# Kernel optimization log

Hardware: AMD Instinct MI355X
Metric: run time of the kernel (lower is better)

Reference implementation:

```python
import jax, jax.numpy as jnp
import numpy as np

N = 50000      # num_nodes
E = 500000     # num_edges
D_IN = 128     # in_features
D_OUT = 128    # out_features
D_REL = 128    # nrela_dim
NEG_SLOPE = 0.2   # LeakyReLU alpha
RATIO = 0.5       # float ratio -> simple (non-schedule) branch
LN_EPS = 1e-5


def setup_inputs() -> dict:
    key = jax.random.key(0)
    ks = jax.random.split(key, 8)
    edge_index = jax.random.randint(ks[0], (2, E), 0, N, dtype=jnp.int64)
    x = jax.random.normal(ks[1], (N, D_IN), dtype=jnp.float32)
    edge_type_embed = jax.random.normal(ks[2], (E, D_REL), dtype=jnp.float32)
    # learned params (xavier-ish scale)
    W = jax.random.normal(ks[3], (4, 2 * D_OUT + D_REL, D_OUT), dtype=jnp.float32) * 0.05
    a = jax.random.normal(ks[4], (4, D_OUT, 1), dtype=jnp.float32) * 0.05
    xw = jax.random.normal(ks[5], (D_IN, D_OUT), dtype=jnp.float32) * (1.0 / np.sqrt(D_IN))
    xb = jnp.zeros((D_OUT,), dtype=jnp.float32)
    gamma = jnp.ones((D_OUT,), dtype=jnp.float32)
    beta = jnp.zeros((D_OUT,), dtype=jnp.float32)
    return {"edge_index": edge_index, "x": x, "edge_type_embed": edge_type_embed,
            "W": W, "a": a, "xw": xw, "xb": xb, "gamma": gamma, "beta": beta}


def _segment_softmax(score, seg, num_segments):
    # per-source-node softmax over edges (matches torch_geometric softmax util)
    seg_max = jax.ops.segment_max(score, seg, num_segments=num_segments)
    seg_max = jnp.where(jnp.isfinite(seg_max), seg_max, 0.0)  # empty segments
    e = jnp.exp(score - seg_max[seg])
    denom = jax.ops.segment_sum(e, seg, num_segments=num_segments)
    return e / (denom[seg] + 1e-16)


def _one_iter(edge_index, xc, ete, Wi, ai):
    src, dst = edge_index[0], edge_index[1]
    # [E, 2*D_OUT + D_REL] @ [2*D_OUT+D_REL, D_OUT] -> [E, D_OUT]
    edge_h = jnp.concatenate([xc[src], xc[dst], ete], axis=1) @ Wi
    score = jax.nn.leaky_relu(jnp.squeeze(edge_h @ ai, -1), NEG_SLOPE)  # [E]
    alpha = _segment_softmax(score, src, N)
    k = int(E * RATIO)
    _, idx = jax.lax.top_k(alpha, k)
    mask = jnp.zeros((E,), dtype=bool).at[idx].set(True)
    alpha = jnp.where(mask, alpha, 0.0)
    # scatter-add weighted messages back to source nodes
    return jax.ops.segment_sum(alpha[:, None] * edge_h, src, num_segments=N)


def reference(edge_index, x, edge_type_embed, W, a, xw, xb, gamma, beta):
    xc = x @ xw + xb  # x_linear
    for i in range(4):  # fixed 4 aggregation iterations (float-ratio branch)
        xc = _one_iter(edge_index, xc, edge_type_embed, W[i], a[i])
    xc = jax.nn.elu(xc)  # concat=True
    mu = jnp.mean(xc, axis=-1, keepdims=True)
    var = jnp.var(xc, axis=-1, keepdims=True)
    return (xc - mu) * jax.lax.rsqrt(var + LN_EPS) * gamma + beta
```

## Files before the change

### kernel.cpp

```cpp
#include <hip/hip_runtime.h>
#include <math.h>

#define DOUT 128

typedef unsigned short u16;
typedef __attribute__((ext_vector_type(8))) short bf16x8;
typedef __attribute__((ext_vector_type(4))) float f32x4;

static __device__ __forceinline__ f32x4 mfma16x16x32(bf16x8 a, bf16x8 b, f32x4 c) {
  return __builtin_amdgcn_mfma_f32_16x16x32_bf16(a, b, c, 0, 0, 0);
}

static __device__ __forceinline__ short bf16i(int v) {
  return (short)(__float_as_uint((float)v) >> 16);
}

static __device__ __forceinline__ float wsum64(float v) {
#pragma unroll
  for (int off = 32; off > 0; off >>= 1) v += __shfl_xor(v, off, 64);
  return v;
}
static __device__ __forceinline__ float wmax64(float v) {
#pragma unroll
  for (int off = 32; off > 0; off >>= 1) v = fmaxf(v, __shfl_xor(v, off, 64));
  return v;
}
static __device__ __forceinline__ float rsumg(float v) {
  v += __shfl_xor(v, 16, 64);
  v += __shfl_xor(v, 32, 64);
  return v;
}

static __device__ __forceinline__ void split3(float x, u16& h, u16& m, u16& l) {
  unsigned u = __float_as_uint(x);
  unsigned rh = u + 0x7FFFu + ((u >> 16) & 1u);
  h = (u16)(rh >> 16);
  float hf = __uint_as_float(rh & 0xFFFF0000u);
  float d1 = x - hf;
  unsigned v = __float_as_uint(d1);
  unsigned rm = v + 0x7FFFu + ((v >> 16) & 1u);
  m = (u16)(rm >> 16);
  float mf = __uint_as_float(rm & 0xFFFF0000u);
  float d2 = d1 - mf;
  unsigned w2 = __float_as_uint(d2);
  unsigned rl = w2 + 0x7FFFu + ((w2 >> 16) & 1u);
  l = (u16)(rl >> 16);
}

static __device__ __forceinline__ void split34(float4 v, uint2& h, uint2& m, uint2& lo) {
  u16 h0, h1, h2, h3, m0, m1, m2, m3, l0, l1, l2, l3;
  split3(v.x, h0, m0, l0);
  split3(v.y, h1, m1, l1);
  split3(v.z, h2, m2, l2);
  split3(v.w, h3, m3, l3);
  h.x = (unsigned)h0 | ((unsigned)h1 << 16);
  h.y = (unsigned)h2 | ((unsigned)h3 << 16);
  m.x = (unsigned)m0 | ((unsigned)m1 << 16);
  m.y = (unsigned)m2 | ((unsigned)m3 << 16);
  lo.x = (unsigned)l0 | ((unsigned)l1 << 16);
  lo.y = (unsigned)l2 | ((unsigned)l3 << 16);
}

__global__ void zero_kernel(int* __restrict__ degcur, unsigned* __restrict__ hists,
                            unsigned* __restrict__ rep, int* __restrict__ candcnt4, int N) {
  int i = blockIdx.x * blockDim.x + threadIdx.x;
  if (i < N) degcur[i] = 0;
  if (i < 4096) hists[i] = 0u;
  if (i < 32768) rep[i] = 0u;
  if (i < 4) candcnt4[i] = 0;
}

__global__ void detect_kernel(const void* __restrict__ ei, int* __restrict__ flag, int E) {
  const int* p = (const int*)ei;
  int lim = (E < 65536) ? E : 65536;
  int i = blockIdx.x * blockDim.x + threadIdx.x;
  int any = 0;
  for (; i < lim; i += gridDim.x * blockDim.x) any |= (p[2 * i + 1] != 0);
  if (__any(any))
    if ((threadIdx.x & 63) == 0 && any) atomicOr(flag, 1);
}

__global__ void cvt_deg_kernel(const void* __restrict__ ei, const int* __restrict__ flag,
                               int* __restrict__ src, int* __restrict__ dst,
                               int* __restrict__ degcur, int E) {
  int i = blockIdx.x * blockDim.x + threadIdx.x;
  if (i >= E) return;
  int s, d;
  if (*flag) { const int* p = (const int*)ei; s = p[i]; d = p[E + i]; }
  else { const long long* p = (const long long*)ei; s = (int)p[i]; d = (int)p[(size_t)E + i]; }
  src[i] = s;
  dst[i] = d;
  atomicAdd(&degcur[s], 1);
}

__global__ void scan_rowptr_kernel(int* __restrict__ degcur, int* __restrict__ rowptr, int N) {
  const int tid = threadIdx.x;
  const int lane = tid & 63, wid = tid >> 6;
  __shared__ int wsumS[16];
  __shared__ int sbase;
  if (tid == 0) sbase = 0;
  __syncthreads();
  for (int base = 0; base < N; base += 1024) {
    int i = base + tid;
    int v = (i < N) ? degcur[i] : 0;
    int x = v;
#pragma unroll
    for (int off = 1; off < 64; off <<= 1) {
      int y = __shfl_up(x, off, 64);
      if (lane >= off) x += y;
    }
    if (lane == 63) wsumS[wid] = x;
    __syncthreads();
    int wbase = 0;
#pragma unroll
    for (int w2 = 0; w2 < 16; ++w2) wbase += (w2 < wid) ? wsumS[w2] : 0;
    int excl = sbase + wbase + x - v;
    if (i < N) { rowptr[i] = excl; degcur[i] = excl; }
    __syncthreads();
    if (tid == 1023) sbase += wbase + x;
    __syncthreads();
  }
  if (tid == 0) rowptr[N] = sbase;
}

__global__ void scatter_kernel(const int* __restrict__ src, int* __restrict__ cursor,
                               int* __restrict__ eids, int E) {
  int e = blockIdx.x * blockDim.x + threadIdx.x;
  if (e >= E) return;
  int p = atomicAdd(&cursor[src[e]], 1);
  eids[p] = e;
}

__global__ void sort_eids_kernel(const int* __restrict__ rowptr, int* __restrict__ eids, int N) {
  int n = blockIdx.x * blockDim.x + threadIdx.x;
  if (n >= N) return;
  int p0 = rowptr[n], p1 = rowptr[n + 1];
  for (int i = p0 + 1; i < p1; ++i) {
    int key = eids[i];
    int j = i - 1;
    while (j >= p0 && eids[j] > key) { eids[j + 1] = eids[j]; --j; }
    eids[j + 1] = key;
  }
}

__global__ void wa_all_kernel(const float* __restrict__ W, const float* __restrict__ a,
                              float* __restrict__ wa_all) {
  int it = blockIdx.x;
  int k = threadIdx.x;
  const float* row = W + ((size_t)it * 384 + k) * DOUT;
  const float* ai = a + (size_t)it * DOUT;
  float acc = 0.f;
  for (int j = 0; j < DOUT; ++j) acc = fmaf(row[j], ai[j], acc);
  wa_all[it * 384 + k] = acc;
}

__global__ void wsplit_kernel(const float* __restrict__ xw, const float* __restrict__ W,
                              u16* __restrict__ wtH, u16* __restrict__ wtM,
                              u16* __restrict__ wtL) {
  __shared__ int muS[32];
  int tid = threadIdx.x;
  {
    int lw = tid & 63, g = lw >> 4;
    bf16x8 aEnc;
#pragma unroll
    for (int j = 0; j < 8; ++j) aEnc[j] = bf16i(8 * g + j + 1);
    f32x4 z = {0.f, 0.f, 0.f, 0.f};
    for (int t0 = 0; t0 < 32; ++t0) {
      int g0 = t0 >> 3, j0 = t0 & 7;
      bf16x8 bOne;
#pragma unroll
      for (int j = 0; j < 8; ++j)
        bOne[j] = (g == g0 && j == j0) ? (short)0x3F80 : (short)0;
      f32x4 d = mfma16x16x32(aEnc, bOne, z);
      if (tid == t0) muS[t0] = ((int)(d[0] + 0.5f) - 1) & 31;
    }
  }
  __syncthreads();
  int b = blockIdx.x;
  int set, ks;
  const float* srcp;
  if (b < 4) { set = 0; ks = b; srcp = xw; }
  else { set = 1 + (b - 4) / 12; ks = (b - 4) % 12; srcp = W + (size_t)(set - 1) * 384 * DOUT; }
  size_t base = ((size_t)set * 12 + ks) * 4096;
  for (int i = tid; i < 4096; i += blockDim.x) {
    int col = i >> 5, t = i & 31;
    float x = srcp[(size_t)(ks * 32 + muS[t]) * DOUT + col];
    u16 h, m, l;
    split3(x, h, m, l);
    wtH[base + i] = h;
    wtM[base + i] = m;
    wtL[base + i] = l;
  }
}

__global__ __launch_bounds__(256) void et4_kernel(const float* __restrict__ ete,
                                                  const float* __restrict__ wa_all,
                                                  float* __restrict__ et4, int E) {
  __shared__ float4 w3s[4][32];
  int tid = threadIdx.x;
  if (tid < 128) {
    int it = tid >> 5, k4 = tid & 31;
    const float* base = wa_all + it * 384 + 256 + k4 * 4;
    w3s[it][k4] = make_float4(base[0], base[1], base[2], base[3]);
  }
  __syncthreads();
  int e = blockIdx.x * blockDim.x + tid;
  if (e >= E) return;
  const float4* row = (const float4*)(ete + (size_t)e * DOUT);
  float a0 = 0.f, a1 = 0.f, a2 = 0.f, a3 = 0.f;
#pragma unroll
  for (int k4 = 0; k4 < 32; ++k4) {
    float4 r = row[k4];
    float4 w0 = w3s[0][k4], w1 = w3s[1][k4], w2 = w3s[2][k4], w3v = w3s[3][k4];
    a0 = fmaf(r.x, w0.x, fmaf(r.y, w0.y, fmaf(r.z, w0.z, fmaf(r.w, w0.w, a0))));
    a1 = fmaf(r.x, w1.x, fmaf(r.y, w1.y, fmaf(r.z, w1.z, fmaf(r.w, w1.w, a1))));
    a2 = fmaf(r.x, w2.x, fmaf(r.y, w2.y, fmaf(r.z, w2.z, fmaf(r.w, w2.w, a2))));
    a3 = fmaf(r.x, w3v.x, fmaf(r.y, w3v.y, fmaf(r.z, w3v.z, fmaf(r.w, w3v.w, a3))));
  }
  et4[e] = a0;
  et4[(size_t)E + e] = a1;
  et4[(size_t)2 * E + e] = a2;
  et4[(size_t)3 * E + e] = a3;
}

__global__ __launch_bounds__(256) void softmax_kernel(
    const int* __restrict__ rowptr, const int* __restrict__ eids, const int* __restrict__ dst,
    const float* __restrict__ pa, const float* __restrict__ qa, const float* __restrict__ et4,
    int it, int E, float* __restrict__ alpha, unsigned* __restrict__ rep0, int N) {
  __shared__ unsigned lh[256];
  int tid = threadIdx.x;
  lh[tid] = 0u;
  __syncthreads();
  const float* etp = et4 + (size_t)it * E;
  int w = (int)(((size_t)blockIdx.x * blockDim.x + tid) >> 6);
  int lane = tid & 63;
  if (w < N) {
    int p0 = rowptr[w], p1 = rowptr[w + 1];
    int deg = p1 - p0;
    if (deg > 0) {
      float pan = pa[w];
      if (deg <= 64) {
        int p = p0 + lane;
        int e = -1;
        float sv = -3.402823466e38f;
        if (p < p1) {
          e = eids[p];
          float s = pan + qa[dst[e]] + etp[e];
          sv = (s >= 0.f) ? s : 0.2f * s;
        }
        float m = wmax64(sv);
        float ee = (e >= 0) ? expf(sv - m) : 0.f;
        float den = 0.f;
        for (int i = 0; i < deg; ++i) den += __shfl(ee, i, 64);
        den += 1e-16f;
        if (e >= 0) {
          float av = ee / den;
          alpha[e] = av;
          atomicAdd(&lh[__float_as_uint(av) >> 24], 1u);
        }
      } else if (deg <= 256) {
        float sv[4]; int ev[4];
#pragma unroll
        for (int u = 0; u < 4; ++u) {
          int p = p0 + u * 64 + lane;
          if (p < p1) {
            int e = eids[p];
            ev[u] = e;
            float s = pan + qa[dst[e]] + etp[e];
            sv[u] = (s >= 0.f) ? s : 0.2f * s;
          } else { ev[u] = -1; sv[u] = -3.402823466e38f; }
        }
        float m = fmaxf(fmaxf(sv[0], sv[1]), fmaxf(sv[2], sv[3]));
        m = wmax64(m);
        float ssum = 0.f;
#pragma unroll
        for (int u = 0; u < 4; ++u)
          if (ev[u] >= 0) { sv[u] = expf(sv[u] - m); ssum += sv[u]; }
        ssum = wsum64(ssum);
        float den = ssum + 1e-16f;
#pragma unroll
        for (int u = 0; u < 4; ++u)
          if (ev[u] >= 0) {
            float av = sv[u] / den;
            alpha[ev[u]] = av;
            atomicAdd(&lh[__float_as_uint(av) >> 24], 1u);
          }
      } else {
        float m = -3.402823466e38f;
        for (int p = p0 + lane; p < p1; p += 64) {
          int e = eids[p];
          float s = pan + qa[dst[e]] + etp[e];
          s = (s >= 0.f) ? s : 0.2f * s;
          m = fmaxf(m, s);
        }
        m = wmax64(m);
        float ssum = 0.f;
        for (int p = p0 + lane; p < p1; p += 64) {
          int e = eids[p];
          float s = pan + qa[dst[e]] + etp[e];
          s = (s >= 0.f) ? s : 0.2f * s;
          ssum += expf(s - m);
        }
        ssum = wsum64(ssum);
        float den = ssum + 1e-16f;
        for (int p = p0 + lane; p < p1; p += 64) {
          int e = eids[p];
          float s = pan + qa[dst[e]] + etp[e];
          s = (s >= 0.f) ? s : 0.2f * s;
          float av = expf(s - m) / den;
          alpha[e] = av;
          atomicAdd(&lh[__float_as_uint(av) >> 24], 1u);
        }
      }
    }
  }
  __syncthreads();
  if (lh[tid]) atomicAdd(&rep0[(blockIdx.x & 31) * 256 + tid], lh[tid]);
}

__device__ __forceinline__ void scan256_step(const unsigned* __restrict__ hist, unsigned krem_in,
                                             unsigned* lds, unsigned* res,
                                             unsigned& bin, unsigned& krem_out) {
  int t = threadIdx.x;
  if (t < 256) lds[t] = hist[t];
  __syncthreads();
  for (int off = 1; off < 256; off <<= 1) {
    unsigned add = 0u;
    if (t < 256 && t + off < 256) add = lds[t + off];
    __syncthreads();
    if (t < 256) lds[t] += add;
    __syncthreads();
  }
  if (t < 256) {
    unsigned above = (t == 255) ? 0u : lds[t + 1];
    if (lds[t] >= krem_in && above < krem_in) { res[0] = (unsigned)t; res[1] = krem_in - above; }
  }
  __syncthreads();
  bin = res[0];
  krem_out = res[1];
  __syncthreads();
}

__device__ __forceinline__ void chain_scan(const unsigned* __restrict__ hists, int upto,
                                           unsigned Ktop, unsigned* lds, unsigned* res,
                                           unsigned& pref, unsigned& krem) {
  pref = 0u; krem = Ktop;
  for (int l = 0; l < upto; ++l) {
    unsigned bin, k2;
    scan256_step(hists + l * 256, krem, lds, res, bin, k2);
    pref |= bin << (24 - 8 * l);
    krem = k2;
  }
}

__global__ __launch_bounds__(256) void hist1_kernel(const float* __restrict__ alpha,
                                                    const unsigned* __restrict__ rep0,
                                                    unsigned* __restrict__ hists_it,
                                                    unsigned Ktop, int E) {
  __shared__ unsigned lds[256], res2[2], lh[256];
  int t = threadIdx.x;
  unsigned v = 0u;
#pragma unroll
  for (int r = 0; r < 32; ++r) v += rep0[r * 256 + t];
  if (blockIdx.x == 0) hists_it[t] = v;
  lds[t] = v;
  __syncthreads();
  for (int off = 1; off < 256; off <<= 1) {
    unsigned add = (t + off < 256) ? lds[t + off] : 0u;
    __syncthreads();
    lds[t] += add;
    __syncthreads();
  }
  {
    unsigned above = (t == 255) ? 0u : lds[t + 1];
    if (lds[t] >= Ktop && above < Ktop) { res2[0] = (unsigned)t; res2[1] = Ktop - above; }
  }
  __syncthreads();
  unsigned bin0 = res2[0];
  lh[t] = 0u;
  __syncthreads();
  unsigned* myh = hists_it + 256;
  for (int e = blockIdx.x * blockDim.x + t; e < E; e += gridDim.x * blockDim.x) {
    unsigned b = __float_as_uint(alpha[e]);
    if ((b >> 24) == bin0) atomicAdd(&lh[(b >> 16) & 0xFFu], 1u);
  }
  __syncthreads();
  if (lh[t]) atomicAdd(&myh[t], lh[t]);
}

__global__ void hist_kernel(const float* __restrict__ alpha, unsigned* __restrict__ hists_it,
                            int level, unsigned Ktop, int E) {
  __shared__ unsigned lds[256], res2[2], lh[256];
  unsigned pref = 0u, krem = Ktop;
  if (level > 0) chain_scan(hists_it, level, Ktop, lds, res2, pref, krem);
  int t = threadIdx.x;
  lh[t] = 0u;
  __syncthreads();
  unsigned* myh = hists_it + level * 256;
  int hs = (level > 0) ? (32 - 8 * level) : 0;
  int bs = 24 - 8 * level;
  for (int e = blockIdx.x * blockDim.x + t; e < E; e += gridDim.x * blockDim.x) {
    unsigned b = __float_as_uint(alpha[e]);
    if (level == 0 || (b >> hs) == (pref >> hs)) atomicAdd(&lh[(b >> bs) & 0xFFu], 1u);
  }
  __syncthreads();
  if (lh[t]) atomicAdd(&myh[t], lh[t]);
}

__global__ void hist3c_kernel(const float* __restrict__ alpha, unsigned* __restrict__ hists_it,
                              unsigned Ktop, int* __restrict__ candList,
                              int* __restrict__ candCnt, int E) {
  __shared__ unsigned lds[256], res2[2], lh[256];
  unsigned pref, krem;
  chain_scan(hists_it, 3, Ktop, lds, res2, pref, krem);
  int t = threadIdx.x;
  lh[t] = 0u;
  __syncthreads();
  unsigned* myh = hists_it + 3 * 256;
  for (int e = blockIdx.x * blockDim.x + t; e < E; e += gridDim.x * blockDim.x) {
    unsigned b = __float_as_uint(alpha[e]);
    if ((b >> 8) == (pref >> 8)) {
      atomicAdd(&lh[b & 0xFFu], 1u);
      int p = atomicAdd(candCnt, 1);
      if (p < 4096) candList[p] = e;
    }
  }
  __syncthreads();
  if (lh[t]) atomicAdd(&myh[t], lh[t]);
}

__global__ __launch_bounds__(1024) void resolve24_kernel(
    const float* __restrict__ alpha, float* __restrict__ amask,
    const unsigned* __restrict__ hists_it, unsigned Ktop,
    const int* __restrict__ candList, const int* __restrict__ candCnt,
    int* __restrict__ header, int E) {
  __shared__ unsigned lds[256], res2[2];
  unsigned thr, needU;
  chain_scan(hists_it, 4, Ktop, lds, res2, thr, needU);
  int needT = (int)needU;
  int cc = *candCnt;
  int tid = threadIdx.x;
  __shared__ int tiel[4096];
  __shared__ int tiec;
  if (tid == 0) tiec = 0;
  __syncthreads();
  if (cc <= 4096) {
    for (int i = tid; i < cc; i += blockDim.x) {
      int e = candList[i];
      if (__float_as_uint(alpha[e]) == thr) { int p = atomicAdd(&tiec, 1); tiel[p] = e; }
    }
    __syncthreads();
    int ce = tiec;
    int dropc = ce - needT;
    if (dropc <= 0) {
      if (tid == 0) { header[0] = 0; header[1] = (int)thr; header[2] = 0; }
      return;
    }
    if (dropc <= 64) {
      int sortN = 64;
      while (sortN < ce) sortN <<= 1;
      for (int i = tid; i < sortN; i += blockDim.x)
        if (i >= ce) tiel[i] = 0x7fffffff;
      __syncthreads();
      for (int k = 2; k <= sortN; k <<= 1) {
        for (int j = k >> 1; j > 0; j >>= 1) {
          for (int i = tid; i < sortN; i += blockDim.x) {
            int ixj = i ^ j;
            if (ixj > i) {
              int v0 = tiel[i], v1 = tiel[ixj];
              bool up = ((i & k) == 0);
              if ((v0 > v1) == up) { tiel[i] = v1; tiel[ixj] = v0; }
            }
          }
          __syncthreads();
        }
      }
      if (tid == 0) { header[0] = 0; header[1] = (int)thr; header[2] = dropc; }
      for (int i = tid; i < dropc; i += blockDim.x) header[3 + i] = tiel[needT + i];
      return;
    }
  }
  if (tid == 0) { header[0] = 1; }
  __shared__ int wtot[16];
  __shared__ int sbase;
  if (tid == 0) sbase = 0;
  __syncthreads();
  int lane = tid & 63, wid = tid >> 6;
  for (int base = 0; base < E; base += 1024) {
    int e = base + tid;
    float a = 0.f; int f = 0; unsigned b = 0u;
    if (e < E) { a = alpha[e]; b = __float_as_uint(a); f = (b == thr) ? 1 : 0; }
    int x = f;
#pragma unroll
    for (int off = 1; off < 64; off <<= 1) {
      int y = __shfl_up(x, off, 64);
      if (lane >= off) x += y;
    }
    if (lane == 63) wtot[wid] = x;
    __syncthreads();
    int wbase = 0;
#pragma unroll
    for (int w2 = 0; w2 < 16; ++w2) wbase += (w2 < wid) ? wtot[w2] : 0;
    if (e < E) {
      float outv = 0.f;
      if (b > thr) outv = a;
      else if (f && (sbase + wbase + x - f) < needT) outv = a;
      amask[e] = outv;
    }
    __syncthreads();
    if (tid == 1023) sbase += wbase + x;
    __syncthreads();
  }
}

static __device__ __forceinline__ float edge_w(const float* __restrict__ alpha,
                                               const float* __restrict__ amask,
                                               const int* __restrict__ hdr, int flg,
                                               unsigned thr, int dc, int e) {
  if (flg) return amask[e];
  float av = alpha[e];
  unsigned b = __float_as_uint(av);
  if (b > thr) return av;
  if (b == thr) {
    for (int j = 0; j < dc; ++j)
      if (hdr[3 + j] == e) return 0.f;
    return av;
  }
  return 0.f;
}

__global__ void agg_kernel(const int* __restrict__ rowptr, const int* __restrict__ eids,
                           const int* __restrict__ dst, const float* __restrict__ alpha,
                           const float* __restrict__ amask, const int* __restrict__ hdr,
                           const float* __restrict__ xc, const float* __restrict__ ete,
                           float* __restrict__ sa, float* __restrict__ vbuf,
                           float* __restrict__ tbuf, int N) {
  int w = (int)(((size_t)blockIdx.x * blockDim.x + threadIdx.x) >> 6);
  int lane = threadIdx.x & 63;
  if (w >= N) return;
  const int flg = hdr[0];
  const unsigned thr = (unsigned)hdr[1];
  const int dc = hdr[2];
  int p0 = rowptr[w], p1 = rowptr[w + 1];
  int deg = p1 - p0;
  const int half = lane >> 5;
  const int l32 = lane & 31;
  const float4* xc4 = (const float4*)xc;
  const float4* et4p = (const float4*)ete;
  float4 acc = make_float4(0.f, 0.f, 0.f, 0.f);
  float s = 0.f;
  if (deg <= 64) {
    int p = p0 + lane;
    int e = -1; float am = 0.f; int dd = 0;
    if (p < p1) { e = eids[p]; am = edge_w(alpha, amask, hdr, flg, thr, dc, e); dd = dst[e]; }
    for (int i = 0; i < deg; ++i) {
      float a = __shfl(am, i, 64);
      if (a != 0.f) {
        int ei = __shfl(e, i, 64);
        int di = __shfl(dd, i, 64);
        const float4* b = half ? (et4p + (size_t)ei * 32) : (xc4 + (size_t)di * 32);
        float4 r = b[l32];
        acc.x = fmaf(a, r.x, acc.x); acc.y = fmaf(a, r.y, acc.y);
        acc.z = fmaf(a, r.z, acc.z); acc.w = fmaf(a, r.w, acc.w);
        s += a;
      }
    }
  } else {
    for (int p = p0; p < p1; ++p) {
      int e0 = eids[p];
      float a0 = edge_w(alpha, amask, hdr, flg, thr, dc, e0);
      if (a0 != 0.f) {
        int d0 = dst[e0];
        const float4* b0 = half ? (et4p + (size_t)e0 * 32) : (xc4 + (size_t)d0 * 32);
        float4 r = b0[l32];
        acc.x = fmaf(a0, r.x, acc.x); acc.y = fmaf(a0, r.y, acc.y);
        acc.z = fmaf(a0, r.z, acc.z); acc.w = fmaf(a0, r.w, acc.w);
        s += a0;
      }
    }
  }
  if (half == 0) ((float4*)vbuf)[(size_t)w * 32 + l32] = acc;
  else           ((float4*)tbuf)[(size_t)w * 32 + l32] = acc;
  if (lane == 0) sa[w] = s;
}

__global__ __launch_bounds__(256) void gemm_mfma_kernel(
    const float* __restrict__ A0, const float* __restrict__ A1, const float* __restrict__ A2,
    const float* __restrict__ sca, const u16* __restrict__ wtH, const u16* __restrict__ wtM,
    const u16* __restrict__ wtL, const float* __restrict__ bias, float* __restrict__ C,
    int N, int nseg,
    const float* __restrict__ wa_next, float* __restrict__ pa, float* __restrict__ qa,
    const float* __restrict__ gamma, const float* __restrict__ beta,
    float* __restrict__ outp, int epi) {
  __shared__ __align__(16) char smem[61440];
  u16 (*AsH)[40] = (u16(*)[40])(smem);
  u16 (*AsM)[40] = (u16(*)[40])(smem + 10240);
  u16 (*AsL)[40] = (u16(*)[40])(smem + 20480);
  u16 (*BsH)[40] = (u16(*)[40])(smem + 30720);
  u16 (*BsM)[40] = (u16(*)[40])(smem + 40960);
  u16 (*BsL)[40] = (u16(*)[40])(smem + 51200);
  const int tid = threadIdx.x;
  const int m0 = blockIdx.x * 128;
  const int K = DOUT * nseg;
  const int w = tid >> 6, l = tid & 63;
  const int cb = l & 15, g = l >> 4;

  int rowlab[4], collab[4];
  {
    bf16x8 enc, ones;
#pragma unroll
    for (int j = 0; j < 8; ++j) { enc[j] = bf16i(cb + 1); ones[j] = (short)0x3F80; }
    f32x4 z = {0.f, 0.f, 0.f, 0.f};
    f32x4 dR = mfma16x16x32(enc, ones, z);
    f32x4 dC = mfma16x16x32(ones, enc, z);
#pragma unroll
    for (int r = 0; r < 4; ++r) {
      rowlab[r] = ((int)(dR[r] * (1.f / 32.f) + 0.5f) - 1) & 15;
      collab[r] = ((int)(dC[r] * (1.f / 32.f) + 0.5f) - 1) & 15;
    }
  }

  f32x4 acc[2][8];
#pragma unroll
  for (int i = 0; i < 2; ++i)
#pragma unroll
    for (int j = 0; j < 8; ++j) acc[i][j] = (f32x4){0.f, 0.f, 0.f, 0.f};

  const int srow = tid >> 1, shalf = tid & 1;
  const int grow_s = m0 + srow;
  float scv = 1.f;
  if (sca && grow_s < N) scv = sca[grow_s];

  for (int kc = 0; kc < K; kc += 32) {
    const int seg = kc >> 7;
    const float* Ap = (seg == 0) ? A0 : (seg == 1) ? A1 : A2;
    float4 v0 = make_float4(0.f, 0.f, 0.f, 0.f), v1 = v0, v2 = v0, v3 = v0;
    if (grow_s < N) {
      const float4* p = (const float4*)(Ap + (size_t)grow_s * DOUT + (kc & 127) + shalf * 16);
      v0 = p[0]; v1 = p[1]; v2 = p[2]; v3 = p[3];
      if (seg == 0 && sca) {
        v0.x *= scv; v0.y *= scv; v0.z *= scv; v0.w *= scv;
        v1.x *= scv; v1.y *= scv; v1.z *= scv; v1.w *= scv;
        v2.x *= scv; v2.y *= scv; v2.z *= scv; v2.w *= scv;
        v3.x *= scv; v3.y *= scv; v3.z *= scv; v3.w *= scv;
      }
    }
    uint2 h0, m0v, l0, h1, m1v, l1, h2, m2v, l2, h3, m3v, l3;
    split34(v0, h0, m0v, l0); split34(v1, h1, m1v, l1);
    split34(v2, h2, m2v, l2); split34(v3, h3, m3v, l3);
    *(uint4*)&AsH[srow][shalf * 16]     = make_uint4(h0.x, h0.y, h1.x, h1.y);
    *(uint4*)&AsH[srow][shalf * 16 + 8] = make_uint4(h2.x, h2.y, h3.x, h3.y);
    *(uint4*)&AsM[srow][shalf * 16]     = make_uint4(m0v.x, m0v.y, m1v.x, m1v.y);
    *(uint4*)&AsM[srow][shalf * 16 + 8] = make_uint4(m2v.x, m2v.y, m3v.x, m3v.y);
    *(uint4*)&AsL[srow][shalf * 16]     = make_uint4(l0.x, l0.y, l1.x, l1.y);
    *(uint4*)&AsL[srow][shalf * 16 + 8] = make_uint4(l2.x, l2.y, l3.x, l3.y);
    {
      size_t sb = (size_t)(kc >> 5) << 12;
      const uint4* gh = (const uint4*)(wtH + sb) + tid * 2;
      const uint4* gm = (const uint4*)(wtM + sb) + tid * 2;
      const uint4* gl = (const uint4*)(wtL + sb) + tid * 2;
      uint4 bh0 = gh[0], bh1 = gh[1];
      uint4 bm0 = gm[0], bm1 = gm[1];
      uint4 bl0 = gl[0], bl1 = gl[1];
      *(uint4*)&BsH[srow][shalf * 16]     = bh0;
      *(uint4*)&BsH[srow][shalf * 16 + 8] = bh1;
      *(uint4*)&BsM[srow][shalf * 16]     = bm0;
      *(uint4*)&BsM[srow][shalf * 16 + 8] = bm1;
      *(uint4*)&BsL[srow][shalf * 16]     = bl0;
      *(uint4*)&BsL[srow][shalf * 16 + 8] = bl1;
    }
    __syncthreads();
    bf16x8 aH0 = *(const bf16x8*)&AsH[w * 32 + cb][g * 8];
    bf16x8 aH1 = *(const bf16x8*)&AsH[w * 32 + 16 + cb][g * 8];
    bf16x8 aM0 = *(const bf16x8*)&AsM[w * 32 + cb][g * 8];
    bf16x8 aM1 = *(const bf16x8*)&AsM[w * 32 + 16 + cb][g * 8];
    bf16x8 aL0 = *(const bf16x8*)&AsL[w * 32 + cb][g * 8];
    bf16x8 aL1 = *(const bf16x8*)&AsL[w * 32 + 16 + cb][g * 8];
#pragma unroll
    for (int ct = 0; ct < 8; ++ct) {
      bf16x8 bH = *(const bf16x8*)&BsH[ct * 16 + cb][g * 8];
      bf16x8 bM = *(const bf16x8*)&BsM[ct * 16 + cb][g * 8];
      bf16x8 bL = *(const bf16x8*)&BsL[ct * 16 + cb][g * 8];
      acc[0][ct] = mfma16x16x32(aH0, bH, acc[0][ct]);
      acc[1][ct] = mfma16x16x32(aH1, bH, acc[1][ct]);
      acc[0][ct] = mfma16x16x32(aM0, bH, acc[0][ct]);
      acc[1][ct] = mfma16x16x32(aM1, bH, acc[1][ct]);
      acc[0][ct] = mfma16x16x32(aL0, bH, acc[0][ct]);
      acc[1][ct] = mfma16x16x32(aL1, bH, acc[1][ct]);
      acc[0][ct] = mfma16x16x32(aH0, bM, acc[0][ct]);
      acc[1][ct] = mfma16x16x32(aH1, bM, acc[1][ct]);
      acc[0][ct] = mfma16x16x32(aM0, bM, acc[0][ct]);
      acc[1][ct] = mfma16x16x32(aM1, bM, acc[1][ct]);
      acc[0][ct] = mfma16x16x32(aH0, bL, acc[0][ct]);
      acc[1][ct] = mfma16x16x32(aH1, bL, acc[1][ct]);
    }
    __syncthreads();
  }

  float* slab = (float*)(smem + (size_t)w * 8448);
  const int row16 = l & 15;
  const int csel = (l >> 4) * 32;
#pragma unroll
  for (int rt = 0; rt < 2; ++rt) {
#pragma unroll
    for (int ct = 0; ct < 8; ++ct)
#pragma unroll
      for (int r = 0; r < 4; ++r)
        slab[rowlab[r] * 132 + ct * 16 + collab[r]] = acc[rt][ct][r];
    __syncthreads();
    int grow = m0 + w * 32 + rt * 16 + row16;
    float v[32];
#pragma unroll
    for (int q = 0; q < 8; ++q) {
      float4 t4 = *(float4*)&slab[row16 * 132 + csel + q * 4];
      v[q * 4 + 0] = t4.x; v[q * 4 + 1] = t4.y; v[q * 4 + 2] = t4.z; v[q * 4 + 3] = t4.w;
    }
    if (bias) {
#pragma unroll
      for (int q = 0; q < 8; ++q) {
        float4 bb = *(const float4*)(bias + csel + q * 4);
        v[q * 4 + 0] += bb.x; v[q * 4 + 1] += bb.y; v[q * 4 + 2] += bb.z; v[q * 4 + 3] += bb.w;
      }
    }
    if (epi == 2) {
#pragma unroll
      for (int i = 0; i < 32; ++i) v[i] = (v[i] > 0.f) ? v[i] : expm1f(v[i]);
      float s = 0.f;
#pragma unroll
      for (int i = 0; i < 32; ++i) s += v[i];
      s = rsumg(s);
      float mu = s * (1.f / 128.f);
      float sq = 0.f;
#pragma unroll
      for (int i = 0; i < 32; ++i) { float d = v[i] - mu; sq += d * d; }
      sq = rsumg(sq);
      float rstd = rsqrtf(sq * (1.f / 128.f) + 1e-5f);
      if (grow < N) {
#pragma unroll
        for (int q = 0; q < 8; ++q) {
          float4 ga = *(const float4*)(gamma + csel + q * 4);
          float4 be = *(const float4*)(beta + csel + q * 4);
          float4 o;
          o.x = (v[q * 4 + 0] - mu) * rstd * ga.x + be.x;
          o.y = (v[q * 4 + 1] - mu) * rstd * ga.y + be.y;
          o.z = (v[q * 4 + 2] - mu) * rstd * ga.z + be.z;
          o.w = (v[q * 4 + 3] - mu) * rstd * ga.w + be.w;
          *(float4*)(outp + (size_t)grow * DOUT + csel + q * 4) = o;
        }
      }
    } else {
      if (grow < N) {
#pragma unroll
        for (int q = 0; q < 8; ++q)
          *(float4*)(C + (size_t)grow * DOUT + csel + q * 4) =
              make_float4(v[q * 4 + 0], v[q * 4 + 1], v[q * 4 + 2], v[q * 4 + 3]);
      }
      if (epi == 1) {
        float pp = 0.f, qq = 0.f;
#pragma unroll
        for (int i = 0; i < 32; ++i) {
          pp = fmaf(v[i], wa_next[csel + i], pp);
          qq = fmaf(v[i], wa_next[128 + csel + i], qq);
        }
        pp = rsumg(pp);
        qq = rsumg(qq);
        if ((l >> 4) == 0 && grow < N) { pa[grow] = pp; qa[grow] = qq; }
      }
    }
    __syncthreads();
  }
}

extern "C" void kernel_launch(void* const* d_in, const int* in_sizes, int n_in,
                              void* d_out, int out_size, void* d_ws, size_t ws_size,
                              hipStream_t stream) {
  const int E = in_sizes[0] / 2;
  const int N = in_sizes[1] / DOUT;
  const unsigned Ktop = (unsigned)(E / 2);

  const void*  ei    = d_in[0];
  const float* x     = (const float*)d_in[1];
  const float* ete   = (const float*)d_in[2];
  const float* W     = (const float*)d_in[3];
  const float* a     = (const float*)d_in[4];
  const float* xw    = (const float*)d_in[5];
  const float* xb    = (const float*)d_in[6];
  const float* gamma = (const float*)d_in[7];
  const float* beta  = (const float*)d_in[8];
  float* out = (float*)d_out;

  size_t off = 0;
  auto take = [&](size_t bytes) -> char* {
    char* p = (char*)d_ws + off;
    off += (bytes + 255) & ~(size_t)255;
    return p;
  };
  int*      src32   = (int*)take((size_t)E * 4);
  int*      dst32   = (int*)take((size_t)E * 4);
  int*      rowptr  = (int*)take(((size_t)N + 1) * 4);
  int*      degcur  = (int*)take((size_t)N * 4);
  int*      eids    = (int*)take((size_t)E * 4);
  float*    pa      = (float*)take((size_t)N * 4);
  float*    qa      = (float*)take((size_t)N * 4);
  float*    wa_all  = (float*)take(4 * 384 * 4);
  float*    alpha   = (float*)take((size_t)E * 4);
  float*    amask   = (float*)take((size_t)E * 4);
  float*    sa      = (float*)take((size_t)N * 4);
  float*    vbuf    = (float*)take((size_t)N * DOUT * 4);
  float*    tbuf    = (float*)take((size_t)N * DOUT * 4);
  float*    xcA     = (float*)take((size_t)N * DOUT * 4);
  float*    xcB     = (float*)take((size_t)N * DOUT * 4);
  float*    et4     = (float*)take((size_t)E * 4 * 4);
  unsigned* hists   = (unsigned*)take(4 * 4 * 256 * 4);
  unsigned* rep     = (unsigned*)take(4 * 32 * 256 * 4);
  int*      candcnt4= (int*)take(64);
  int*      flag    = (int*)take(64);
  int*      candList= (int*)take(4096 * 4);
  int*      header  = (int*)take(4 * 80 * 4);
  u16*      wtH     = (u16*)take((size_t)5 * 12 * 4096 * 2);
  u16*      wtM     = (u16*)take((size_t)5 * 12 * 4096 * 2);
  u16*      wtL     = (u16*)take((size_t)5 * 12 * 4096 * 2);
  (void)ws_size; (void)n_in; (void)out_size;

  const int TB  = 256;
  const int gE  = (E + TB - 1) / TB;
  const int gN  = (N + TB - 1) / TB;
  const int gN4 = (N + 3) / 4;
  const int gM  = (N + 127) / 128;

  (void)hipMemsetAsync(flag, 0, 4, stream);
  zero_kernel<<<gN, TB, 0, stream>>>(degcur, hists, rep, candcnt4, N);
  detect_kernel<<<64, TB, 0, stream>>>(ei, flag, E);
  cvt_deg_kernel<<<gE, TB, 0, stream>>>(ei, flag, src32, dst32, degcur, E);
  scan_rowptr_kernel<<<1, 1024, 0, stream>>>(degcur, rowptr, N);
  scatter_kernel<<<gE, TB, 0, stream>>>(src32, degcur, eids, E);
  sort_eids_kernel<<<gN, TB, 0, stream>>>(rowptr, eids, N);
  wa_all_kernel<<<4, 384, 0, stream>>>(W, a, wa_all);
  wsplit_kernel<<<52, 256, 0, stream>>>(xw, W, wtH, wtM, wtL);
  et4_kernel<<<gE, TB, 0, stream>>>(ete, wa_all, et4, E);
  gemm_mfma_kernel<<<gM, 256, 0, stream>>>(x, nullptr, nullptr, nullptr, wtH, wtM, wtL, xb,
                                           xcA, N, 1, wa_all, pa, qa, nullptr, nullptr,
                                           nullptr, 1);

  float* bufs[2] = {xcA, xcB};
  for (int it = 0; it < 4; ++it) {
    const float* xc = bufs[it & 1];
    float* xn = bufs[(it & 1) ^ 1];
    unsigned* hists_it = hists + it * 1024;
    unsigned* rep_it = rep + it * 8192;
    int* hdr_it = header + it * 80;
    const u16* wH = wtH + (size_t)(it + 1) * 12 * 4096;
    const u16* wM = wtM + (size_t)(it + 1) * 12 * 4096;
    const u16* wL = wtL + (size_t)(it + 1) * 12 * 4096;

    softmax_kernel<<<gN4, TB, 0, stream>>>(rowptr, eids, dst32, pa, qa, et4, it, E, alpha,
                                           rep_it, N);
    hist1_kernel<<<384, 256, 0, stream>>>(alpha, rep_it, hists_it, Ktop, E);
    hist_kernel<<<384, 256, 0, stream>>>(alpha, hists_it, 2, Ktop, E);
    hist3c_kernel<<<384, 256, 0, stream>>>(alpha, hists_it, Ktop, candList,
                                           candcnt4 + it, E);
    resolve24_kernel<<<1, 1024, 0, stream>>>(alpha, amask, hists_it, Ktop, candList,
                                             candcnt4 + it, hdr_it, E);
    agg_kernel<<<gN4, TB, 0, stream>>>(rowptr, eids, dst32, alpha, amask, hdr_it,
                                       xc, ete, sa, vbuf, tbuf, N);
    if (it < 3)
      gemm_mfma_kernel<<<gM, 256, 0, stream>>>(xc, vbuf, tbuf, sa, wH, wM, wL, nullptr, xn,
                                               N, 3, wa_all + (it + 1) * 384, pa, qa,
                                               nullptr, nullptr, nullptr, 1);
    else
      gemm_mfma_kernel<<<gM, 256, 0, stream>>>(xc, vbuf, tbuf, sa, wH, wM, wL, nullptr, xn,
                                               N, 3, nullptr, pa, qa, gamma, beta, out, 2);
  }
}
```

Baseline: 903.3 us.

## Prefetch GEMM tiles, use packed bf16 split conversion, merge setup kernels

The MFMA GEMM main loop now loads the next K-chunk of A and B into registers before the MFMA work on the current chunk, so global-load latency overlaps with compute. The three-way bf16 split of the A operand now uses the hardware packed conversion instruction v_cvt_pk_bf16_f32 instead of manual integer rounding. Separately, the zero and detect setup kernels are merged into one launch, as are the wa and wsplit weight-prep kernels, to cut launch count. In exchange the loop holds more live registers, which may lower occupancy.

After: 884.0 us. 2.1% less time.

```diff
diff --git a/kernel.cpp b/kernel.cpp
--- a/kernel.cpp
+++ b/kernel.cpp
@@ -47,35 +47,36 @@
   l = (u16)(rl >> 16);
 }
 
-static __device__ __forceinline__ void split34(float4 v, uint2& h, uint2& m, uint2& lo) {
-  u16 h0, h1, h2, h3, m0, m1, m2, m3, l0, l1, l2, l3;
-  split3(v.x, h0, m0, l0);
-  split3(v.y, h1, m1, l1);
-  split3(v.z, h2, m2, l2);
-  split3(v.w, h3, m3, l3);
-  h.x = (unsigned)h0 | ((unsigned)h1 << 16);
-  h.y = (unsigned)h2 | ((unsigned)h3 << 16);
-  m.x = (unsigned)m0 | ((unsigned)m1 << 16);
-  m.y = (unsigned)m2 | ((unsigned)m3 << 16);
-  lo.x = (unsigned)l0 | ((unsigned)l1 << 16);
-  lo.y = (unsigned)l2 | ((unsigned)l3 << 16);
-}
-
-__global__ void zero_kernel(int* __restrict__ degcur, unsigned* __restrict__ hists,
-                            unsigned* __restrict__ rep, int* __restrict__ candcnt4, int N) {
+static __device__ __forceinline__ void split3pk(float x0, float x1,
+                                                unsigned& h, unsigned& m, unsigned& l) {
+  unsigned hp, mp, lp;
+  asm("v_cvt_pk_bf16_f32 %0, %1, %2" : "=v"(hp) : "v"(x0), "v"(x1));
+  float d0 = x0 - __uint_as_float(hp << 16);
+  float d1 = x1 - __uint_as_float(hp & 0xFFFF0000u);
+  asm("v_cvt_pk_bf16_f32 %0, %1, %2" : "=v"(mp) : "v"(d0), "v"(d1));
+  float e0 = d0 - __uint_as_float(mp << 16);
+  float e1 = d1 - __uint_as_float(mp & 0xFFFF0000u);
+  asm("v_cvt_pk_bf16_f32 %0, %1, %2" : "=v"(lp) : "v"(e0), "v"(e1));
+  h = hp; m = mp; l = lp;
+}
+static __device__ __forceinline__ void split34pk(float4 v, uint2& h, uint2& m, uint2& lo) {
+  split3pk(v.x, v.y, h.x, m.x, lo.x);
+  split3pk(v.z, v.w, h.y, m.y, lo.y);
+}
+
+__global__ void zero_detect_kernel(int* __restrict__ degcur, unsigned* __restrict__ hists,
+                                   unsigned* __restrict__ rep, int* __restrict__ candcnt4,
+                                   int N, const void* __restrict__ ei, int* __restrict__ flag,
+                                   int E) {
   int i = blockIdx.x * blockDim.x + threadIdx.x;
   if (i < N) degcur[i] = 0;
   if (i < 4096) hists[i] = 0u;
   if (i < 32768) rep[i] = 0u;
   if (i < 4) candcnt4[i] = 0;
-}
-
-__global__ void detect_kernel(const void* __restrict__ ei, int* __restrict__ flag, int E) {
   const int* p = (const int*)ei;
   int lim = (E < 65536) ? E : 65536;
-  int i = blockIdx.x * blockDim.x + threadIdx.x;
   int any = 0;
-  for (; i < lim; i += gridDim.x * blockDim.x) any |= (p[2 * i + 1] != 0);
+  for (int j = i; j < lim; j += gridDim.x * blockDim.x) any |= (p[2 * j + 1] != 0);
   if (__any(any))
     if ((threadIdx.x & 63) == 0 && any) atomicOr(flag, 1);
 }
@@ -143,22 +144,22 @@
   }
 }
 
-__global__ void wa_all_kernel(const float* __restrict__ W, const float* __restrict__ a,
-                              float* __restrict__ wa_all) {
-  int it = blockIdx.x;
-  int k = threadIdx.x;
-  const float* row = W + ((size_t)it * 384 + k) * DOUT;
-  const float* ai = a + (size_t)it * DOUT;
-  float acc = 0.f;
-  for (int j = 0; j < DOUT; ++j) acc = fmaf(row[j], ai[j], acc);
-  wa_all[it * 384 + k] = acc;
-}
-
-__global__ void wsplit_kernel(const float* __restrict__ xw, const float* __restrict__ W,
-                              u16* __restrict__ wtH, u16* __restrict__ wtM,
-                              u16* __restrict__ wtL) {
+__global__ void wprep_kernel(const float* __restrict__ W, const float* __restrict__ a,
+                             float* __restrict__ wa_all, const float* __restrict__ xw,
+                             u16* __restrict__ wtH, u16* __restrict__ wtM,
+                             u16* __restrict__ wtL) {
+  int blk = blockIdx.x;
+  int tid = threadIdx.x;
+  if (blk < 4) {
+    int it = blk, k = tid;
+    const float* row = W + ((size_t)it * 384 + k) * DOUT;
+    const float* ai = a + (size_t)it * DOUT;
+    float acc = 0.f;
+    for (int j = 0; j < DOUT; ++j) acc = fmaf(row[j], ai[j], acc);
+    wa_all[it * 384 + k] = acc;
+    return;
+  }
   __shared__ int muS[32];
-  int tid = threadIdx.x;
   {
     int lw = tid & 63, g = lw >> 4;
     bf16x8 aEnc;
@@ -176,7 +177,7 @@
     }
   }
   __syncthreads();
-  int b = blockIdx.x;
+  int b = blk - 4;
   int set, ks;
   const float* srcp;
   if (b < 4) { set = 0; ks = b; srcp = xw; }
@@ -631,10 +632,10 @@
   float scv = 1.f;
   if (sca && grow_s < N) scv = sca[grow_s];
 
-  for (int kc = 0; kc < K; kc += 32) {
+  auto loadA = [&](int kc, float4& v0, float4& v1, float4& v2, float4& v3) {
     const int seg = kc >> 7;
     const float* Ap = (seg == 0) ? A0 : (seg == 1) ? A1 : A2;
-    float4 v0 = make_float4(0.f, 0.f, 0.f, 0.f), v1 = v0, v2 = v0, v3 = v0;
+    v0 = make_float4(0.f, 0.f, 0.f, 0.f); v1 = v0; v2 = v0; v3 = v0;
     if (grow_s < N) {
       const float4* p = (const float4*)(Ap + (size_t)grow_s * DOUT + (kc & 127) + shalf * 16);
       v0 = p[0]; v1 = p[1]; v2 = p[2]; v3 = p[3];
@@ -645,29 +646,46 @@
         v3.x *= scv; v3.y *= scv; v3.z *= scv; v3.w *= scv;
       }
     }
-    uint2 h0, m0v, l0, h1, m1v, l1, h2, m2v, l2, h3, m3v, l3;
-    split34(v0, h0, m0v, l0); split34(v1, h1, m1v, l1);
-    split34(v2, h2, m2v, l2); split34(v3, h3, m3v, l3);
-    *(uint4*)&AsH[srow][shalf * 16]     = make_uint4(h0.x, h0.y, h1.x, h1.y);
-    *(uint4*)&AsH[srow][shalf * 16 + 8] = make_uint4(h2.x, h2.y, h3.x, h3.y);
-    *(uint4*)&AsM[srow][shalf * 16]     = make_uint4(m0v.x, m0v.y, m1v.x, m1v.y);
-    *(uint4*)&AsM[srow][shalf * 16 + 8] = make_uint4(m2v.x, m2v.y, m3v.x, m3v.y);
-    *(uint4*)&AsL[srow][shalf * 16]     = make_uint4(l0.x, l0.y, l1.x, l1.y);
-    *(uint4*)&AsL[srow][shalf * 16 + 8] = make_uint4(l2.x, l2.y, l3.x, l3.y);
+  };
+  auto loadB = [&](int kc, uint4& h0, uint4& h1, uint4& m0u, uint4& m1u, uint4& l0u,
+                   uint4& l1u) {
+    size_t sb = (size_t)(kc >> 5) << 12;
+    const uint4* gh = (const uint4*)(wtH + sb) + tid * 2;
+    const uint4* gm = (const uint4*)(wtM + sb) + tid * 2;
+    const uint4* gl = (const uint4*)(wtL + sb) + tid * 2;
+    h0 = gh[0]; h1 = gh[1];
+    m0u = gm[0]; m1u = gm[1];
+    l0u = gl[0]; l1u = gl[1];
+  };
+
+  float4 av0, av1, av2, av3, nv0, nv1, nv2, nv3;
+  uint4 bh0, bh1, bm0u, bm1u, bl0u, bl1u, nh0, nh1, nm0, nm1, nl0, nl1;
+  loadA(0, av0, av1, av2, av3);
+  loadB(0, bh0, bh1, bm0u, bm1u, bl0u, bl1u);
+
+  const int nks = K >> 5;
+  for (int ks = 0; ks < nks; ++ks) {
+    const int kc = ks << 5;
     {
-      size_t sb = (size_t)(kc >> 5) << 12;
-      const uint4* gh = (const uint4*)(wtH + sb) + tid * 2;
-      const uint4* gm = (const uint4*)(wtM + sb) + tid * 2;
-      const uint4* gl = (const uint4*)(wtL + sb) + tid * 2;
-      uint4 bh0 = gh[0], bh1 = gh[1];
-      uint4 bm0 = gm[0], bm1 = gm[1];
-      uint4 bl0 = gl[0], bl1 = gl[1];
+      uint2 h0, m0v, l0, h1, m1v, l1, h2, m2v, l2, h3, m3v, l3;
+      split34pk(av0, h0, m0v, l0); split34pk(av1, h1, m1v, l1);
+      split34pk(av2, h2, m2v, l2); split34pk(av3, h3, m3v, l3);
+      *(uint4*)&AsH[srow][shalf * 16]     = make_uint4(h0.x, h0.y, h1.x, h1.y);
+      *(uint4*)&AsH[srow][shalf * 16 + 8] = make_uint4(h2.x, h2.y, h3.x, h3.y);
+      *(uint4*)&AsM[srow][shalf * 16]     = make_uint4(m0v.x, m0v.y, m1v.x, m1v.y);
+      *(uint4*)&AsM[srow][shalf * 16 + 8] = make_uint4(m2v.x, m2v.y, m3v.x, m3v.y);
+      *(uint4*)&AsL[srow][shalf * 16]     = make_uint4(l0.x, l0.y, l1.x, l1.y);
+      *(uint4*)&AsL[srow][shalf * 16 + 8] = make_uint4(l2.x, l2.y, l3.x, l3.y);
       *(uint4*)&BsH[srow][shalf * 16]     = bh0;
       *(uint4*)&BsH[srow][shalf * 16 + 8] = bh1;
-      *(uint4*)&BsM[srow][shalf * 16]     = bm0;
-      *(uint4*)&BsM[srow][shalf * 16 + 8] = bm1;
-      *(uint4*)&BsL[srow][shalf * 16]     = bl0;
-      *(uint4*)&BsL[srow][shalf * 16 + 8] = bl1;
+      *(uint4*)&BsM[srow][shalf * 16]     = bm0u;
+      *(uint4*)&BsM[srow][shalf * 16 + 8] = bm1u;
+      *(uint4*)&BsL[srow][shalf * 16]     = bl0u;
+      *(uint4*)&BsL[srow][shalf * 16 + 8] = bl1u;
+    }
+    if (ks + 1 < nks) {
+      loadA(kc + 32, nv0, nv1, nv2, nv3);
+      loadB(kc + 32, nh0, nh1, nm0, nm1, nl0, nl1);
     }
     __syncthreads();
     bf16x8 aH0 = *(const bf16x8*)&AsH[w * 32 + cb][g * 8];
@@ -695,6 +713,8 @@
       acc[1][ct] = mfma16x16x32(aH1, bL, acc[1][ct]);
     }
     __syncthreads();
+    av0 = nv0; av1 = nv1; av2 = nv2; av3 = nv3;
+    bh0 = nh0; bh1 = nh1; bm0u = nm0; bm1u = nm1; bl0u = nl0; bl1u = nl1;
   }
 
   float* slab = (float*)(smem + (size_t)w * 8448);
@@ -829,14 +849,12 @@
   const int gM  = (N + 127) / 128;
 
   (void)hipMemsetAsync(flag, 0, 4, stream);
-  zero_kernel<<<gN, TB, 0, stream>>>(degcur, hists, rep, candcnt4, N);
-  detect_kernel<<<64, TB, 0, stream>>>(ei, flag, E);
+  zero_detect_kernel<<<gN, TB, 0, stream>>>(degcur, hists, rep, candcnt4, N, ei, flag, E);
   cvt_deg_kernel<<<gE, TB, 0, stream>>>(ei, flag, src32, dst32, degcur, E);
   scan_rowptr_kernel<<<1, 1024, 0, stream>>>(degcur, rowptr, N);
   scatter_kernel<<<gE, TB, 0, stream>>>(src32, degcur, eids, E);
   sort_eids_kernel<<<gN, TB, 0, stream>>>(rowptr, eids, N);
-  wa_all_kernel<<<4, 384, 0, stream>>>(W, a, wa_all);
-  wsplit_kernel<<<52, 256, 0, stream>>>(xw, W, wtH, wtM, wtL);
+  wprep_kernel<<<56, 384, 0, stream>>>(W, a, wa_all, xw, wtH, wtM, wtL);
   et4_kernel<<<gE, TB, 0, stream>>>(ete, wa_all, et4, E);
   gemm_mfma_kernel<<<gM, 256, 0, stream>>>(x, nullptr, nullptr, nullptr, wtH, wtM, wtL, xb,
                                            xcA, N, 1, wa_all, pa, qa, nullptr, nullptr,
```
